# Optimization experiments

Measured on AMD Instinct MI355X. Metric: run time of the kernel, lower is better.

## Reference

```python
import jax, jax.numpy as jnp
import numpy as np

L = 5        # num_layer
D = 128      # emb_dim
N = 100000   # nodes
E = 500000   # edges
G = 128      # graphs in batch
NUM_TYPES = 100
NUM_ATTRS = 1000
MAX_DEPTH = 21


def _bn(x, g, b):
    # training-mode BatchNorm1d statistics (per-feature over rows)
    mu = x.mean(axis=0)
    var = x.var(axis=0)
    return (x - mu) * jax.lax.rsqrt(var + 1e-5) * g + b


def setup_inputs() -> dict:
    key = jax.random.key(0)
    ks = jax.random.split(key, 24)
    inp = {}
    x0 = jax.random.randint(ks[0], (N,), 0, NUM_TYPES)
    x1 = jax.random.randint(ks[1], (N,), 0, NUM_ATTRS)
    inp['x'] = jnp.stack([x0, x1], axis=1)
    inp['node_depth'] = jax.random.randint(ks[2], (N,), 0, MAX_DEPTH)
    inp['edge_index'] = jax.random.randint(ks[3], (2, E), 0, N)
    inp['batch'] = jnp.sort(jax.random.randint(ks[4], (N,), 0, G))
    inp['edge_attr'] = jax.random.normal(ks[5], (E, 2), dtype=jnp.float32)
    s = 0.02
    inp['type_emb'] = jax.random.normal(ks[6], (NUM_TYPES, D), dtype=jnp.float32) * s
    inp['attr_emb'] = jax.random.normal(ks[7], (NUM_ATTRS, D), dtype=jnp.float32) * s
    inp['depth_emb'] = jax.random.normal(ks[8], (MAX_DEPTH, D), dtype=jnp.float32) * s
    inp['vn_emb'] = jnp.zeros((1, D), dtype=jnp.float32)  # init constant 0
    inp['eps'] = jnp.zeros((L,), dtype=jnp.float32)       # GIN eps
    inp['edge_W'] = jax.random.normal(ks[9], (L, 2, D), dtype=jnp.float32) * s
    inp['edge_b'] = jnp.zeros((L, D), dtype=jnp.float32)
    inp['gin_W1'] = jax.random.normal(ks[10], (L, D, 2 * D), dtype=jnp.float32) * s
    inp['gin_b1'] = jnp.zeros((L, 2 * D), dtype=jnp.float32)
    inp['gin_bng'] = jnp.ones((L, 2 * D), dtype=jnp.float32)
    inp['gin_bnb'] = jnp.zeros((L, 2 * D), dtype=jnp.float32)
    inp['gin_W2'] = jax.random.normal(ks[11], (L, 2 * D, D), dtype=jnp.float32) * s
    inp['gin_b2'] = jnp.zeros((L, D), dtype=jnp.float32)
    inp['bng'] = jnp.ones((L, D), dtype=jnp.float32)
    inp['bnb'] = jnp.zeros((L, D), dtype=jnp.float32)
    inp['vn_W1'] = jax.random.normal(ks[12], (L - 1, D, 2 * D), dtype=jnp.float32) * s
    inp['vn_b1'] = jnp.zeros((L - 1, 2 * D), dtype=jnp.float32)
    inp['vn_bn1g'] = jnp.ones((L - 1, 2 * D), dtype=jnp.float32)
    inp['vn_bn1b'] = jnp.zeros((L - 1, 2 * D), dtype=jnp.float32)
    inp['vn_W2'] = jax.random.normal(ks[13], (L - 1, 2 * D, D), dtype=jnp.float32) * s
    inp['vn_b2'] = jnp.zeros((L - 1, D), dtype=jnp.float32)
    inp['vn_bn2g'] = jnp.ones((L - 1, D), dtype=jnp.float32)
    inp['vn_bn2b'] = jnp.zeros((L - 1, D), dtype=jnp.float32)
    return inp


def reference(x, node_depth, edge_index, batch, edge_attr,
              type_emb, attr_emb, depth_emb, vn_emb, eps,
              edge_W, edge_b, gin_W1, gin_b1, gin_bng, gin_bnb, gin_W2, gin_b2,
              bng, bnb, vn_W1, vn_b1, vn_bn1g, vn_bn1b, vn_W2, vn_b2, vn_bn2g, vn_bn2b):
    # node encoder: type + attribute + depth embeddings  -> [N, D]
    h = type_emb[x[:, 0]] + attr_emb[x[:, 1]] + depth_emb[node_depth]
    vn = jnp.broadcast_to(vn_emb[0], (G, D))  # virtual node per graph
    src, dst = edge_index[0], edge_index[1]
    for l in range(L):
        # broadcast virtual node to its graph's nodes
        h = h + vn[batch]
        # GIN conv: aggr_j relu(h_j + edge_emb), then (1+eps)*h + aggr -> MLP
        eemb = edge_attr @ edge_W[l] + edge_b[l]            # [E, D]
        msg = jax.nn.relu(h[src] + eemb)                    # [E, D]
        aggr = jax.ops.segment_sum(msg, dst, num_segments=N)
        z = (1.0 + eps[l]) * h + aggr
        z = jax.nn.relu(_bn(z @ gin_W1[l] + gin_b1[l], gin_bng[l], gin_bnb[l]))
        z = z @ gin_W2[l] + gin_b2[l]
        hn = _bn(z, bng[l], bnb[l])                         # outer BatchNorm
        if l < L - 1:
            hn = jax.nn.relu(hn)                            # dropout=identity (eval)
            # virtual node update: global_add_pool of pre-conv h + MLP
            vt = jax.ops.segment_sum(h, batch, num_segments=G) + vn
            vt = jax.nn.relu(_bn(vt @ vn_W1[l] + vn_b1[l], vn_bn1g[l], vn_bn1b[l]))
            vn = jax.nn.relu(_bn(vt @ vn_W2[l] + vn_b2[l], vn_bn2g[l], vn_bn2b[l]))
        h = hn
    return h  # JK == 'last'
```

## Files before the change

kernel.cpp:

```cpp
#include <hip/hip_runtime.h>

#define D 128
#define GG 128
#define SLOTS 64

typedef __attribute__((ext_vector_type(8))) short bf16x8;
typedef __attribute__((ext_vector_type(4))) float f32x4;

__device__ __forceinline__ short f2bf(float f) {
  unsigned u = __float_as_uint(f);
  unsigned r = u + 0x7fffu + ((u >> 16) & 1u);
  return (short)(r >> 16);
}
__device__ __forceinline__ float bf2f(unsigned short h) {
  return __uint_as_float(((unsigned)h) << 16);
}

__device__ __forceinline__ void bn_coef(float s, float q, float invn, float g, float b,
                                        float& sc, float& sh) {
  float mu = s * invn;
  float var = q * invn - mu * mu;
  sc = g * rsqrtf(var + 1e-5f);
  sh = b - mu * sc;
}

__global__ void k_deg(int E, const int* __restrict__ dst, int* __restrict__ deg) {
  int e = blockIdx.x * 256 + threadIdx.x;
  if (e < E) atomicAdd(&deg[dst[e]], 1);
}

__global__ void k_scan1(int N, const int* __restrict__ deg,
                        int* __restrict__ incl, int* __restrict__ blksum) {
  __shared__ int s[256];
  int t = threadIdx.x, n = blockIdx.x * 256 + t;
  int v = (n < N) ? ((deg[n] + 3) & ~3) : 0;
  s[t] = v; __syncthreads();
  for (int off = 1; off < 256; off <<= 1) {
    int x = (t >= off) ? s[t - off] : 0;
    __syncthreads();
    s[t] += x;
    __syncthreads();
  }
  if (n < N) incl[n] = s[t];
  if (t == 255) blksum[blockIdx.x] = s[255];
}

__global__ void k_scan2(int B, int* __restrict__ blksum) {
  __shared__ int s[512];
  int t = threadIdx.x;
  s[t] = (t < B) ? blksum[t] : 0;
  __syncthreads();
  for (int off = 1; off < 512; off <<= 1) {
    int x = (t >= off) ? s[t - off] : 0;
    __syncthreads();
    s[t] += x;
    __syncthreads();
  }
  if (t < B) blksum[t] = s[t];
}

__global__ void k_scan3(int N, const int* __restrict__ incl, const int* __restrict__ blksum,
                        const int* __restrict__ deg, int* __restrict__ row_ptr) {
  int n = blockIdx.x * 256 + threadIdx.x;
  if (n >= N) return;
  int b = n >> 8;
  int off = (b > 0) ? blksum[b - 1] : 0;
  int pdeg = (deg[n] + 3) & ~3;
  row_ptr[n] = off + incl[n] - pdeg;
  if (n == N - 1) row_ptr[N] = off + incl[n];
}

__global__ void k_fill(int E, const int* __restrict__ src, const int* __restrict__ dst,
                       const float* __restrict__ ea, const int* __restrict__ row_ptr,
                       int* __restrict__ cursor, int4* __restrict__ er) {
  int e = blockIdx.x * 256 + threadIdx.x;
  if (e >= E) return;
  int d = dst[e];
  int pos = row_ptr[d] + atomicAdd(&cursor[d], 1);
  er[pos] = make_int4(src[e] << 8, __float_as_int(ea[2 * e]), __float_as_int(ea[2 * e + 1]), 0);
}

__global__ void k_padfill(int N, const int* __restrict__ deg, const int* __restrict__ row_ptr,
                          int4* __restrict__ er) {
  int n = blockIdx.x * 256 + threadIdx.x;
  if (n >= N) return;
  int s = row_ptr[n] + deg[n], e = row_ptr[n + 1];
  int4 pad = make_int4(N << 8, 0, 0, 0);
  for (int p = s; p < e; ++p) er[p] = pad;
}

__global__ void k_sentinel(int N, short* __restrict__ h2) {
  h2[(size_t)N * D + threadIdx.x] = f2bf(-1e30f);
}

__global__ void k_pack(const float* __restrict__ gW1, const float* __restrict__ gW2,
                       short* __restrict__ w1t, short* __restrict__ w2t) {
  int id = blockIdx.x * 256 + threadIdx.x;
  if (id < 5 * 256 * 128) {
    int l = id / 32768, r = id % 32768, n = r / 128, k = r % 128;
    w1t[id] = f2bf(gW1[l * 32768 + k * 256 + n]);
  }
  if (id < 5 * 128 * 256) {
    int l = id / 32768, r = id % 32768, n = r / 256, k = r % 256;
    w2t[id] = f2bf(gW2[l * 32768 + k * 128 + n]);
  }
}

__global__ void k_coef(int NC,
                       const float* __restrict__ part_s, const float* __restrict__ part_q,
                       float* __restrict__ outs, float* __restrict__ outq) {
  int t = threadIdx.x;
  if (t >= NC) return;
  float s = 0.f, q = 0.f;
  #pragma unroll 4
  for (int i = 0; i < SLOTS; ++i) {
    s += part_s[i * NC + t];
    q += part_q[i * NC + t];
  }
  outs[t] = s; outq[t] = q;
}

__global__ void k_nodeprep(int N, int mode,
    const int* __restrict__ x, const int* __restrict__ depth,
    const float* __restrict__ te, const float* __restrict__ ae, const float* __restrict__ de,
    const short* __restrict__ z2, const float* __restrict__ s2, const float* __restrict__ q2,
    const float* __restrict__ g2, const float* __restrict__ b2,
    int vn_mode, const float* __restrict__ vne,
    const float* __restrict__ t2v, const float* __restrict__ vs2, const float* __restrict__ vq2,
    const float* __restrict__ vg2, const float* __restrict__ vb2,
    const int* __restrict__ batch,
    short* __restrict__ h2, float* __restrict__ vt_pool, int do_pool)
{
  int t = threadIdx.x;
  int d0 = (t & 63) * 2;
  int grp = t >> 6;
  int n0 = blockIdx.x * 32 + grp * 8;
  float invn = 1.0f / (float)N;
  float sc0 = 0.f, sh0 = 0.f, sc1 = 0.f, sh1 = 0.f;
  float vsc0 = 0.f, vsh0 = 0.f, vsc1 = 0.f, vsh1 = 0.f;
  if (mode == 1) {
    bn_coef(s2[d0], q2[d0], invn, g2[d0], b2[d0], sc0, sh0);
    bn_coef(s2[d0 + 1], q2[d0 + 1], invn, g2[d0 + 1], b2[d0 + 1], sc1, sh1);
  }
  if (vn_mode == 1) {
    bn_coef(vs2[d0], vq2[d0], 1.0f / (float)GG, vg2[d0], vb2[d0], vsc0, vsh0);
    bn_coef(vs2[d0 + 1], vq2[d0 + 1], 1.0f / (float)GG, vg2[d0 + 1], vb2[d0 + 1], vsc1, vsh1);
  }
  int cur = -1; float a0 = 0.f, a1 = 0.f;
  for (int k = 0; k < 8; ++k) {
    int n = n0 + k;
    if (n >= N) break;
    float h0, h1;
    if (mode == 0) {
      int x0 = x[2 * n], x1 = x[2 * n + 1], dp = depth[n];
      float2 e0 = *(const float2*)(te + (size_t)x0 * D + d0);
      float2 e1 = *(const float2*)(ae + (size_t)x1 * D + d0);
      float2 e2 = *(const float2*)(de + (size_t)dp * D + d0);
      h0 = e0.x + e1.x + e2.x;
      h1 = e0.y + e1.y + e2.y;
    } else {
      unsigned zv = *(const unsigned*)(z2 + (size_t)n * D + d0);
      h0 = fmaxf(bf2f((unsigned short)(zv & 0xffff)) * sc0 + sh0, 0.f);
      h1 = fmaxf(bf2f((unsigned short)(zv >> 16))    * sc1 + sh1, 0.f);
    }
    int g = batch[n];
    float v0, v1;
    if (vn_mode == 0) { v0 = vne[d0]; v1 = vne[d0 + 1]; }
    else {
      float2 tv = *(const float2*)(t2v + (size_t)g * D + d0);
      v0 = fmaxf(tv.x * vsc0 + vsh0, 0.f);
      v1 = fmaxf(tv.y * vsc1 + vsh1, 0.f);
    }
    h0 += v0; h1 += v1;
    unsigned o = ((unsigned)(unsigned short)f2bf(h0)) |
                 (((unsigned)(unsigned short)f2bf(h1)) << 16);
    *(unsigned*)(h2 + (size_t)n * D + d0) = o;
    if (do_pool) {
      if (g != cur) {
        if (cur >= 0) {
          atomicAdd(&vt_pool[cur * D + d0], a0);
          atomicAdd(&vt_pool[cur * D + d0 + 1], a1);
        }
        cur = g; a0 = 0.f; a1 = 0.f;
      }
      a0 += h0; a1 += h1;
    }
  }
  if (do_pool && cur >= 0) {
    atomicAdd(&vt_pool[cur * D + d0], a0);
    atomicAdd(&vt_pool[cur * D + d0 + 1], a1);
  }
}

__global__ void __launch_bounds__(256) k_gather(int N,
    const int* __restrict__ row_ptr, const int4* __restrict__ er,
    const float* __restrict__ ew, const float* __restrict__ eb,
    const float* __restrict__ epsp,
    const short* __restrict__ h2, short* __restrict__ am)
{
  int t = threadIdx.x;
  int w = t >> 6, l = t & 63;
  int n = blockIdx.x * 4 + w;
  if (n >= N) return;
  const char* h2b = (const char*)h2;
  int lb = l << 2;
  int d0 = l * 2;
  float ew00 = ew[d0], ew01 = ew[d0 + 1];
  float ew10 = ew[D + d0], ew11 = ew[D + d0 + 1];
  float eb0 = eb[d0], eb1 = eb[d0 + 1];
  float ep1 = 1.0f + epsp[0];
  unsigned hv = *(const unsigned*)(h2b + ((size_t)n << 8) + lb);
  float acc0 = ep1 * bf2f((unsigned short)(hv & 0xffff));
  float acc1 = ep1 * bf2f((unsigned short)(hv >> 16));
  int beg = row_ptr[n], end = row_ptr[n + 1];
  for (int i = beg; i < end; i += 4) {
    int4 e0 = er[i], e1 = er[i + 1], e2 = er[i + 2], e3 = er[i + 3];
    unsigned v0 = *(const unsigned*)(h2b + e0.x + lb);
    unsigned v1 = *(const unsigned*)(h2b + e1.x + lb);
    unsigned v2 = *(const unsigned*)(h2b + e2.x + lb);
    unsigned v3 = *(const unsigned*)(h2b + e3.x + lb);
    float a0x = __int_as_float(e0.y), a0y = __int_as_float(e0.z);
    float a1x = __int_as_float(e1.y), a1y = __int_as_float(e1.z);
    float a2x = __int_as_float(e2.y), a2y = __int_as_float(e2.z);
    float a3x = __int_as_float(e3.y), a3y = __int_as_float(e3.z);
    acc0 += fmaxf(bf2f((unsigned short)(v0 & 0xffff)) + a0x * ew00 + a0y * ew10 + eb0, 0.f);
    acc1 += fmaxf(bf2f((unsigned short)(v0 >> 16))    + a0x * ew01 + a0y * ew11 + eb1, 0.f);
    acc0 += fmaxf(bf2f((unsigned short)(v1 & 0xffff)) + a1x * ew00 + a1y * ew10 + eb0, 0.f);
    acc1 += fmaxf(bf2f((unsigned short)(v1 >> 16))    + a1x * ew01 + a1y * ew11 + eb1, 0.f);
    acc0 += fmaxf(bf2f((unsigned short)(v2 & 0xffff)) + a2x * ew00 + a2y * ew10 + eb0, 0.f);
    acc1 += fmaxf(bf2f((unsigned short)(v2 >> 16))    + a2x * ew01 + a2y * ew11 + eb1, 0.f);
    acc0 += fmaxf(bf2f((unsigned short)(v3 & 0xffff)) + a3x * ew00 + a3y * ew10 + eb0, 0.f);
    acc1 += fmaxf(bf2f((unsigned short)(v3 >> 16))    + a3x * ew01 + a3y * ew11 + eb1, 0.f);
  }
  unsigned o = ((unsigned)(unsigned short)f2bf(acc0)) |
               (((unsigned)(unsigned short)f2bf(acc1)) << 16);
  *(unsigned*)(am + (size_t)n * D + d0) = o;
}

template<int STAGES, int BN_A>
__global__ void __launch_bounds__(256, 4) k_gemm(int N, int NC, float invn,
    const short* __restrict__ A, int strideA,
    const short* __restrict__ Bt, int strideB,
    const float* __restrict__ bias,
    const float* __restrict__ pAs, const float* __restrict__ pAq,
    const float* __restrict__ gam, const float* __restrict__ bet,
    short* __restrict__ C, int strideC,
    float* __restrict__ part_s, float* __restrict__ part_q)
{
  __shared__ __align__(16) char As[32768];
  __shared__ float scs[256], shs[256];
  __shared__ float cs[128], cq[128];
  int t = threadIdx.x;
  int m0 = blockIdx.x * 128;
  int n0 = blockIdx.y * 128;
  int w = t >> 6, l = t & 63;
  int wr = w >> 1, wc = w & 1;
  int lm = l & 15, kb = l >> 4;

  if (t < 128) { cs[t] = 0.f; cq[t] = 0.f; }
  if (BN_A) {
    float s = 0.f, q = 0.f;
    #pragma unroll 8
    for (int i = 0; i < SLOTS; ++i) {
      s += pAs[i * 256 + t];
      q += pAq[i * 256 + t];
    }
    float a, c;
    bn_coef(s, q, invn, gam[t], bet[t], a, c);
    scs[t] = a; shs[t] = c;
  }
  __syncthreads();

  f32x4 acc[4][4];
  #pragma unroll
  for (int j = 0; j < 4; ++j) {
    float bj = bias[n0 + wc * 64 + j * 16 + lm];
    #pragma unroll
    for (int i = 0; i < 4; ++i) acc[i][j] = (f32x4){bj, bj, bj, bj};
  }

  #pragma unroll
  for (int s = 0; s < STAGES; ++s) {
    if (s > 0) __syncthreads();
    #pragma unroll
    for (int r = 0; r < 8; ++r) {
      int p = (r * 256 + t) * 16;
      int row = p >> 8, c = p & 255;
      int gr = m0 + row; if (gr > N - 1) gr = N - 1;
      bf16x8 v = *(const bf16x8*)((const char*)A + (size_t)gr * strideA + s * 256 + c);
      if (BN_A) {
        int kg = s * 128 + (c >> 1);
        float4 s0 = *(const float4*)(scs + kg);
        float4 s1 = *(const float4*)(scs + kg + 4);
        float4 h0 = *(const float4*)(shs + kg);
        float4 h1 = *(const float4*)(shs + kg + 4);
        v[0] = f2bf(fmaxf(bf2f((unsigned short)v[0]) * s0.x + h0.x, 0.f));
        v[1] = f2bf(fmaxf(bf2f((unsigned short)v[1]) * s0.y + h0.y, 0.f));
        v[2] = f2bf(fmaxf(bf2f((unsigned short)v[2]) * s0.z + h0.z, 0.f));
        v[3] = f2bf(fmaxf(bf2f((unsigned short)v[3]) * s0.w + h0.w, 0.f));
        v[4] = f2bf(fmaxf(bf2f((unsigned short)v[4]) * s1.x + h1.x, 0.f));
        v[5] = f2bf(fmaxf(bf2f((unsigned short)v[5]) * s1.y + h1.y, 0.f));
        v[6] = f2bf(fmaxf(bf2f((unsigned short)v[6]) * s1.z + h1.z, 0.f));
        v[7] = f2bf(fmaxf(bf2f((unsigned short)v[7]) * s1.w + h1.w, 0.f));
      }
      *(bf16x8*)(As + row * 256 + (c ^ ((row & 7) << 4))) = v;
    }
    __syncthreads();
    #pragma unroll
    for (int ks = 0; ks < 4; ++ks) {
      int kB = ks * 64 + kb * 16;
      bf16x8 fa[4], fb[4];
      #pragma unroll
      for (int j = 0; j < 4; ++j) {
        int cl = n0 + wc * 64 + j * 16 + lm;
        fb[j] = *(const bf16x8*)((const char*)Bt + (size_t)cl * strideB + s * 256 + kB);
      }
      #pragma unroll
      for (int i = 0; i < 4; ++i) {
        int rl = wr * 64 + i * 16 + lm;
        fa[i] = *(const bf16x8*)(As + rl * 256 + (kB ^ ((rl & 7) << 4)));
      }
      #pragma unroll
      for (int i = 0; i < 4; ++i)
        #pragma unroll
        for (int j = 0; j < 4; ++j)
          acc[i][j] = __builtin_amdgcn_mfma_f32_16x16x32_bf16(fa[i], fb[j], acc[i][j], 0, 0, 0);
    }
  }

  #pragma unroll
  for (int j = 0; j < 4; ++j) {
    int col = wc * 64 + j * 16 + lm;
    float sv = 0.f, qv = 0.f;
    #pragma unroll
    for (int i = 0; i < 4; ++i) {
      #pragma unroll
      for (int r = 0; r < 4; ++r) {
        int row = m0 + wr * 64 + i * 16 + kb * 4 + r;
        float vv = acc[i][j][r];
        if (row < N) { sv += vv; qv += vv * vv; }
      }
    }
    sv += __shfl_xor(sv, 16); sv += __shfl_xor(sv, 32);
    qv += __shfl_xor(qv, 16); qv += __shfl_xor(qv, 32);
    if (l < 16) { atomicAdd(&cs[col], sv); atomicAdd(&cq[col], qv); }
  }
  __syncthreads();
  if (t < 128) {
    int slot = (blockIdx.x + blockIdx.y) & (SLOTS - 1);
    atomicAdd(&part_s[(size_t)slot * NC + n0 + t], cs[t]);
    atomicAdd(&part_q[(size_t)slot * NC + n0 + t], cq[t]);
  }

  #pragma unroll
  for (int j = 0; j < 4; ++j) {
    int colb = (wc * 64 + j * 16 + lm) * 2;
    #pragma unroll
    for (int i = 0; i < 4; ++i) {
      int rowb = wr * 64 + i * 16 + kb * 4;
      #pragma unroll
      for (int r = 0; r < 4; ++r) {
        int row = rowb + r;
        *(short*)(As + row * 256 + (colb ^ ((row & 7) << 4))) = f2bf(acc[i][j][r]);
      }
    }
  }
  __syncthreads();
  {
    int tr = t >> 1, half = t & 1;
    int grow = m0 + tr;
    if (grow < N) {
      #pragma unroll
      for (int u = 0; u < 8; ++u) {
        int off = half * 128 + u * 16;
        bf16x8 v = *(const bf16x8*)(As + tr * 256 + (off ^ ((tr & 7) << 4)));
        *(bf16x8*)(C + (size_t)grow * strideC + n0 + half * 64 + u * 8) = v;
      }
    }
  }
}

__global__ void k_vn1(const float* __restrict__ vt_pool,
    int vn_mode, const float* __restrict__ vne, const float* __restrict__ t2v,
    const float* __restrict__ vs2, const float* __restrict__ vq2,
    const float* __restrict__ vg2, const float* __restrict__ vb2,
    const float* __restrict__ W1, const float* __restrict__ b1,
    float* __restrict__ t1v, float* __restrict__ s1, float* __restrict__ q1)
{
  __shared__ float vrow[128];
  int g = blockIdx.x, t = threadIdx.x;
  if (t < 128) {
    float vnv;
    if (vn_mode == 0) vnv = vne[t];
    else {
      float sc, sh;
      bn_coef(vs2[t], vq2[t], 1.f / (float)GG, vg2[t], vb2[t], sc, sh);
      vnv = fmaxf(t2v[g * D + t] * sc + sh, 0.f);
    }
    vrow[t] = vt_pool[g * D + t] + vnv;
  }
  __syncthreads();
  float acc = b1[t];
  for (int k = 0; k < 128; ++k) acc += vrow[k] * W1[k * 256 + t];
  t1v[g * 256 + t] = acc;
  atomicAdd(&s1[t], acc);
  atomicAdd(&q1[t], acc * acc);
}

__global__ void k_vn2(const float* __restrict__ t1v,
    const float* __restrict__ s1, const float* __restrict__ q1,
    const float* __restrict__ g1, const float* __restrict__ b1bn,
    const float* __restrict__ W2, const float* __restrict__ b2,
    float* __restrict__ t2v, float* __restrict__ s2, float* __restrict__ q2)
{
  __shared__ float p[256];
  int g = blockIdx.x, t = threadIdx.x;
  for (int u = t; u < 256; u += 128) {
    float sc, sh;
    bn_coef(s1[u], q1[u], 1.f / (float)GG, g1[u], b1bn[u], sc, sh);
    p[u] = fmaxf(t1v[g * 256 + u] * sc + sh, 0.f);
  }
  __syncthreads();
  float acc = b2[t];
  for (int k = 0; k < 256; ++k) acc += p[k] * W2[k * D + t];
  t2v[g * D + t] = acc;
  atomicAdd(&s2[t], acc);
  atomicAdd(&q2[t], acc * acc);
}

__global__ void k_out(int N, const short* __restrict__ z2,
    const float* __restrict__ s2, const float* __restrict__ q2,
    const float* __restrict__ g2, const float* __restrict__ b2, float* __restrict__ out)
{
  long long idx = (long long)blockIdx.x * 256 + threadIdx.x;
  long long base = idx * 2;
  if (base >= (long long)N * D) return;
  int d = (int)(base & (D - 1));
  float invn = 1.f / (float)N;
  unsigned v = *(const unsigned*)(z2 + base);
  float sc0, sh0, sc1, sh1;
  bn_coef(s2[d], q2[d], invn, g2[d], b2[d], sc0, sh0);
  bn_coef(s2[d + 1], q2[d + 1], invn, g2[d + 1], b2[d + 1], sc1, sh1);
  out[base]     = bf2f((unsigned short)(v & 0xffff)) * sc0 + sh0;
  out[base + 1] = bf2f((unsigned short)(v >> 16))    * sc1 + sh1;
}

extern "C" void kernel_launch(void* const* d_in, const int* in_sizes, int n_in,
                              void* d_out, int out_size, void* d_ws, size_t ws_size,
                              hipStream_t stream) {
  const int*   x     = (const int*)d_in[0];
  const int*   depth = (const int*)d_in[1];
  const int*   eidx  = (const int*)d_in[2];
  const int*   batch = (const int*)d_in[3];
  const float* ea    = (const float*)d_in[4];
  const float* te    = (const float*)d_in[5];
  const float* aemb  = (const float*)d_in[6];
  const float* de    = (const float*)d_in[7];
  const float* vne   = (const float*)d_in[8];
  const float* epsp  = (const float*)d_in[9];
  const float* eW    = (const float*)d_in[10];
  const float* eb    = (const float*)d_in[11];
  const float* gW1   = (const float*)d_in[12];
  const float* gb1   = (const float*)d_in[13];
  const float* gbng  = (const float*)d_in[14];
  const float* gbnb  = (const float*)d_in[15];
  const float* gW2   = (const float*)d_in[16];
  const float* gb2   = (const float*)d_in[17];
  const float* bng   = (const float*)d_in[18];
  const float* bnb   = (const float*)d_in[19];
  const float* vW1   = (const float*)d_in[20];
  const float* vb1   = (const float*)d_in[21];
  const float* vbn1g = (const float*)d_in[22];
  const float* vbn1b = (const float*)d_in[23];
  const float* vW2   = (const float*)d_in[24];
  const float* vb2   = (const float*)d_in[25];
  const float* vbn2g = (const float*)d_in[26];
  const float* vbn2b = (const float*)d_in[27];

  int N = in_sizes[0] / 2;
  int E = in_sizes[2] / 2;
  const int* src = eidx;
  const int* dst = eidx + E;

  char* wsp = (char*)d_ws;
  auto alloc = [&](size_t bytes) -> char* {
    char* p = wsp; wsp += (bytes + 15) & ~(size_t)15; return p;
  };
  short* h2         = (short*)alloc((size_t)(N + 1) * 128 * 2);
  short* am         = (short*)alloc((size_t)N * 128 * 2);
  short* t1         = (short*)alloc((size_t)N * 256 * 2);
  short* z2         = (short*)alloc((size_t)N * 128 * 2);
  short* w1t        = (short*)alloc((size_t)5 * 256 * 128 * 2);
  short* w2t        = (short*)alloc((size_t)5 * 128 * 256 * 2);
  int*   row_ptr    = (int*)alloc((size_t)(N + 1) * 4);
  int*   incl       = (int*)alloc((size_t)N * 4);
  int*   blksum     = (int*)alloc(512 * 4);
  int4*  er         = (int4*)alloc(((size_t)E + 3 * (size_t)N + 16) * 16);
  char* zero_base = wsp;
  int*  deg    = (int*)alloc((size_t)N * 4);
  int*  cursor = (int*)alloc((size_t)N * 4);
  float* sp = (float*)wsp;
  float *p1s[5], *p1q[5], *p2s[5], *p2q[5], *s2s[5], *q2s[5];
  for (int l = 0; l < 5; ++l) {
    p1s[l]=sp; sp+=SLOTS*256; p1q[l]=sp; sp+=SLOTS*256;
    p2s[l]=sp; sp+=SLOTS*128; p2q[l]=sp; sp+=SLOTS*128;
    s2s[l]=sp; sp+=128; q2s[l]=sp; sp+=128;
  }
  float *vt[4], *t1v[4], *t2v[4], *vs1[4], *vq1[4], *vs2[4], *vq2[4];
  for (int l = 0; l < 4; ++l) {
    vt[l]=sp;  sp+=GG*D;
    t1v[l]=sp; sp+=GG*256;
    t2v[l]=sp; sp+=GG*D;
    vs1[l]=sp; sp+=256; vq1[l]=sp; sp+=256;
    vs2[l]=sp; sp+=128; vq2[l]=sp; sp+=128;
  }
  size_t zero_bytes = (size_t)((char*)sp - zero_base);
  hipMemsetAsync(zero_base, 0, zero_bytes, stream);

  int eblk = (E + 255) / 256;
  int nblk = (N + 255) / 256;
  int B = nblk;
  k_deg<<<eblk, 256, 0, stream>>>(E, dst, deg);
  k_scan1<<<nblk, 256, 0, stream>>>(N, deg, incl, blksum);
  k_scan2<<<1, 512, 0, stream>>>(B, blksum);
  k_scan3<<<nblk, 256, 0, stream>>>(N, incl, blksum, deg, row_ptr);
  k_fill<<<eblk, 256, 0, stream>>>(E, src, dst, ea, row_ptr, cursor, er);
  k_padfill<<<nblk, 256, 0, stream>>>(N, deg, row_ptr, er);
  k_sentinel<<<1, 128, 0, stream>>>(N, h2);

  k_pack<<<(5 * 256 * 128 + 255) / 256, 256, 0, stream>>>(gW1, gW2, w1t, w2t);

  int nblk_a = (N + 31) / 32;
  int nblk_gth = (N + 3) / 4;
  int nblk_m = (N + 127) / 128;
  float invn = 1.f / (float)N;

  for (int l = 0; l < 5; ++l) {
    int mode    = (l == 0) ? 0 : 1;
    int vn_mode = (l == 0) ? 0 : 1;
    int do_pool = (l < 4) ? 1 : 0;
    const float* ps2  = (l > 0) ? s2s[l-1] : s2s[0];
    const float* pq2  = (l > 0) ? q2s[l-1] : q2s[0];
    const float* pg2  = (l > 0) ? bng + (l-1)*D : bng;
    const float* pb2  = (l > 0) ? bnb + (l-1)*D : bnb;
    const float* pt2v = (l > 0) ? t2v[l-1] : t2v[0];
    const float* pvs2 = (l > 0) ? vs2[l-1] : vs2[0];
    const float* pvq2 = (l > 0) ? vq2[l-1] : vq2[0];
    const float* pvg2 = (l > 0) ? vbn2g + (l-1)*D : vbn2g;
    const float* pvb2 = (l > 0) ? vbn2b + (l-1)*D : vbn2b;

    k_nodeprep<<<nblk_a, 256, 0, stream>>>(N, mode, x, depth, te, aemb, de,
        z2, ps2, pq2, pg2, pb2,
        vn_mode, vne, pt2v, pvs2, pvq2, pvg2, pvb2,
        batch, h2, do_pool ? vt[l] : vt[0], do_pool);

    k_gather<<<nblk_gth, 256, 0, stream>>>(N, row_ptr, er,
        eW + l*2*D, eb + l*D, epsp + l, h2, am);

    k_gemm<1, 0><<<dim3(nblk_m, 2), 256, 0, stream>>>(N, 256, invn,
        am, 256, w1t + (size_t)l*256*128, 256,
        gb1 + l*256, nullptr, nullptr, nullptr, nullptr,
        t1, 256, p1s[l], p1q[l]);

    k_gemm<2, 1><<<dim3(nblk_m, 1), 256, 0, stream>>>(N, 128, invn,
        t1, 512, w2t + (size_t)l*128*256, 512,
        gb2 + l*128, p1s[l], p1q[l], gbng + l*256, gbnb + l*256,
        z2, 128, p2s[l], p2q[l]);

    k_coef<<<1, 128, 0, stream>>>(128, p2s[l], p2q[l], s2s[l], q2s[l]);

    if (l < 4) {
      k_vn1<<<GG, 256, 0, stream>>>(vt[l], vn_mode, vne, pt2v, pvs2, pvq2, pvg2, pvb2,
          vW1 + (size_t)l*128*256, vb1 + l*256, t1v[l], vs1[l], vq1[l]);
      k_vn2<<<GG, 128, 0, stream>>>(t1v[l], vs1[l], vq1[l],
          vbn1g + l*256, vbn1b + l*256,
          vW2 + (size_t)l*256*128, vb2 + l*128, t2v[l], vs2[l], vq2[l]);
    }
  }

  k_out<<<(int)(((long long)N * D / 2 + 255) / 256), 256, 0, stream>>>(N, z2, s2s[4], q2s[4],
      bng + 4*D, bnb + 4*D, (float*)d_out);
}
```

Before: 987.0 us.

## Use direct global-to-LDS loads, register prefetch for BN path, coalesced output stores

For the non-BN GEMM path, A tiles are loaded straight into LDS with global_load_lds, applying the swizzle on the source address and skipping the register round trip. For the BN path, the next stage's A tile is prefetched into registers while the current stage is transformed. The epilogue store is remapped so 16 threads write each full row contiguously, giving coalesced global writes. The aim is fewer VGPR staging cycles and better overlap of memory latency, at the cost of extra registers for the prefetch buffer.

```diff
diff --git a/kernel.cpp b/kernel.cpp
--- a/kernel.cpp
+++ b/kernel.cpp
@@ -6,6 +6,8 @@
 
 typedef __attribute__((ext_vector_type(8))) short bf16x8;
 typedef __attribute__((ext_vector_type(4))) float f32x4;
+typedef __attribute__((address_space(1))) const unsigned gas_u32;
+typedef __attribute__((address_space(3))) unsigned las_u32;
 
 __device__ __forceinline__ short f2bf(float f) {
   unsigned u = __float_as_uint(f);
@@ -279,16 +281,36 @@
     for (int i = 0; i < 4; ++i) acc[i][j] = (f32x4){bj, bj, bj, bj};
   }
 
-  #pragma unroll
-  for (int s = 0; s < STAGES; ++s) {
-    if (s > 0) __syncthreads();
+  bf16x8 pre[8];
+  if (BN_A) {
     #pragma unroll
     for (int r = 0; r < 8; ++r) {
       int p = (r * 256 + t) * 16;
       int row = p >> 8, c = p & 255;
       int gr = m0 + row; if (gr > N - 1) gr = N - 1;
-      bf16x8 v = *(const bf16x8*)((const char*)A + (size_t)gr * strideA + s * 256 + c);
-      if (BN_A) {
+      pre[r] = *(const bf16x8*)((const char*)A + (size_t)gr * strideA + 0 * 256 + c);
+    }
+  }
+
+  #pragma unroll
+  for (int s = 0; s < STAGES; ++s) {
+    if (s > 0) __syncthreads();
+    if (!BN_A) {
+      #pragma unroll
+      for (int r = 0; r < 8; ++r) {
+        int p = (r * 256 + t) * 16;
+        int row = p >> 8, csw = p & 255;
+        int c = csw ^ ((row & 7) << 4);
+        int gr = m0 + row; if (gr > N - 1) gr = N - 1;
+        const char* gsrc = (const char*)A + (size_t)gr * strideA + s * 256 + c;
+        __builtin_amdgcn_global_load_lds((gas_u32*)gsrc, (las_u32*)(As + p), 16, 0, 0);
+      }
+    } else {
+      #pragma unroll
+      for (int r = 0; r < 8; ++r) {
+        int p = (r * 256 + t) * 16;
+        int row = p >> 8, c = p & 255;
+        bf16x8 v = pre[r];
         int kg = s * 128 + (c >> 1);
         float4 s0 = *(const float4*)(scs + kg);
         float4 s1 = *(const float4*)(scs + kg + 4);
@@ -302,8 +324,17 @@
         v[5] = f2bf(fmaxf(bf2f((unsigned short)v[5]) * s1.y + h1.y, 0.f));
         v[6] = f2bf(fmaxf(bf2f((unsigned short)v[6]) * s1.z + h1.z, 0.f));
         v[7] = f2bf(fmaxf(bf2f((unsigned short)v[7]) * s1.w + h1.w, 0.f));
-      }
-      *(bf16x8*)(As + row * 256 + (c ^ ((row & 7) << 4))) = v;
+        *(bf16x8*)(As + row * 256 + (c ^ ((row & 7) << 4))) = v;
+      }
+      if (s + 1 < STAGES) {
+        #pragma unroll
+        for (int r = 0; r < 8; ++r) {
+          int p = (r * 256 + t) * 16;
+          int row = p >> 8, c = p & 255;
+          int gr = m0 + row; if (gr > N - 1) gr = N - 1;
+          pre[r] = *(const bf16x8*)((const char*)A + (size_t)gr * strideA + (s + 1) * 256 + c);
+        }
+      }
     }
     __syncthreads();
     #pragma unroll
@@ -367,15 +398,15 @@
   }
   __syncthreads();
   {
-    int tr = t >> 1, half = t & 1;
-    int grow = m0 + tr;
-    if (grow < N) {
-      #pragma unroll
-      for (int u = 0; u < 8; ++u) {
-        int off = half * 128 + u * 16;
-        bf16x8 v = *(const bf16x8*)(As + tr * 256 + (off ^ ((tr & 7) << 4)));
-        *(bf16x8*)(C + (size_t)grow * strideC + n0 + half * 64 + u * 8) = v;
-      }
+    int rr = t >> 4, ck = t & 15;
+    #pragma unroll
+    for (int it = 0; it < 8; ++it) {
+      int row = it * 16 + rr;
+      int grow = m0 + row;
+      int off = ck * 16;
+      bf16x8 v = *(const bf16x8*)(As + row * 256 + (off ^ ((row & 7) << 4)));
+      if (grow < N)
+        *(bf16x8*)(C + (size_t)grow * strideC + n0 + ck * 8) = v;
     }
   }
 }
```

After: 1.018 ms. 1.03x slower.

## Retile MLP GEMMs to 64-row full-width blocks and fuse virtual-node kernels

Applied to the files above, without the earlier changes.

The first GEMM now computes all 256 output columns per 64-row block, so each A tile is read once instead of once per column half. The second GEMM also drops to 64-row tiles, which roughly doubles the block count. The BN coefficients for the hidden layer are now computed once in a separate k_coef launch rather than re-reduced from 64 slots in every GEMM block. The two virtual-node MLP kernels are merged into one, with an atomic-counter grid barrier across 128 blocks. That merge relies on all blocks being co-resident and adds a spin-wait, and it also adds one extra small kernel launch per layer.

```diff
diff --git a/kernel.cpp b/kernel.cpp
--- a/kernel.cpp
+++ b/kernel.cpp
@@ -106,8 +106,10 @@
   }
 }
 
-__global__ void k_coef(int NC,
+__global__ void k_coef(int NC, float invn,
                        const float* __restrict__ part_s, const float* __restrict__ part_q,
+                       const float* __restrict__ g, const float* __restrict__ b,
+                       float* __restrict__ sc, float* __restrict__ sh,
                        float* __restrict__ outs, float* __restrict__ outq) {
   int t = threadIdx.x;
   if (t >= NC) return;
@@ -117,7 +119,12 @@
     s += part_s[i * NC + t];
     q += part_q[i * NC + t];
   }
-  outs[t] = s; outq[t] = q;
+  if (outs) { outs[t] = s; outq[t] = q; }
+  if (g) {
+    float a, c;
+    bn_coef(s, q, invn, g[t], b[t], a, c);
+    sc[t] = a; sh[t] = c;
+  }
 }
 
 __global__ void k_nodeprep(int N, int mode,
@@ -237,91 +244,184 @@
   *(unsigned*)(am + (size_t)n * D + d0) = o;
 }
 
-template<int STAGES, int BN_A>
-__global__ void __launch_bounds__(256, 4) k_gemm(int N, int NC, float invn,
-    const short* __restrict__ A, int strideA,
-    const short* __restrict__ Bt, int strideB,
+__global__ void __launch_bounds__(256) k_gemm1(int N,
+    const short* __restrict__ A, const short* __restrict__ Bt,
     const float* __restrict__ bias,
-    const float* __restrict__ pAs, const float* __restrict__ pAq,
-    const float* __restrict__ gam, const float* __restrict__ bet,
-    short* __restrict__ C, int strideC,
+    short* __restrict__ C,
     float* __restrict__ part_s, float* __restrict__ part_q)
 {
-  __shared__ __align__(16) char As[32768];
+  __shared__ __align__(16) char As[16384];
+  __shared__ float cs[256], cq[256];
+  int t = threadIdx.x;
+  int m0 = blockIdx.x * 64;
+  int w = t >> 6, l = t & 63;
+  int wr = w >> 1, wc = w & 1;
+  int lm = l & 15, kb = l >> 4;
+  cs[t] = 0.f; cq[t] = 0.f;
+
+  f32x4 acc[2][8];
+  #pragma unroll
+  for (int j = 0; j < 8; ++j) {
+    float bj = bias[wc * 128 + j * 16 + lm];
+    acc[0][j] = (f32x4){bj, bj, bj, bj};
+    acc[1][j] = (f32x4){bj, bj, bj, bj};
+  }
+
+  #pragma unroll
+  for (int r = 0; r < 4; ++r) {
+    int p = (r * 256 + t) * 16;
+    int row = p >> 8, c = p & 255;
+    int gr = m0 + row; if (gr > N - 1) gr = N - 1;
+    bf16x8 v = *(const bf16x8*)((const char*)A + (size_t)gr * 256 + c);
+    *(bf16x8*)(As + row * 256 + (c ^ ((row & 7) << 4))) = v;
+  }
+  __syncthreads();
+  #pragma unroll
+  for (int ks = 0; ks < 4; ++ks) {
+    int kB = ks * 64 + kb * 16;
+    bf16x8 fa[2], fb[8];
+    #pragma unroll
+    for (int j = 0; j < 8; ++j) {
+      int cl = wc * 128 + j * 16 + lm;
+      fb[j] = *(const bf16x8*)((const char*)Bt + (size_t)cl * 256 + kB);
+    }
+    #pragma unroll
+    for (int i = 0; i < 2; ++i) {
+      int rl = wr * 32 + i * 16 + lm;
+      fa[i] = *(const bf16x8*)(As + rl * 256 + (kB ^ ((rl & 7) << 4)));
+    }
+    #pragma unroll
+    for (int i = 0; i < 2; ++i)
+      #pragma unroll
+      for (int j = 0; j < 8; ++j)
+        acc[i][j] = __builtin_amdgcn_mfma_f32_16x16x32_bf16(fa[i], fb[j], acc[i][j], 0, 0, 0);
+  }
+
+  #pragma unroll
+  for (int j = 0; j < 8; ++j) {
+    int col = wc * 128 + j * 16 + lm;
+    float sv = 0.f, qv = 0.f;
+    #pragma unroll
+    for (int i = 0; i < 2; ++i) {
+      #pragma unroll
+      for (int r = 0; r < 4; ++r) {
+        int row = m0 + wr * 32 + i * 16 + kb * 4 + r;
+        float vv = acc[i][j][r];
+        if (row < N) { sv += vv; qv += vv * vv; }
+      }
+    }
+    sv += __shfl_xor(sv, 16); sv += __shfl_xor(sv, 32);
+    qv += __shfl_xor(qv, 16); qv += __shfl_xor(qv, 32);
+    if (l < 16) { atomicAdd(&cs[col], sv); atomicAdd(&cq[col], qv); }
+  }
+  __syncthreads();
+  {
+    int slot = blockIdx.x & (SLOTS - 1);
+    atomicAdd(&part_s[(size_t)slot * 256 + t], cs[t]);
+    atomicAdd(&part_q[(size_t)slot * 256 + t], cq[t]);
+  }
+
+  #pragma unroll
+  for (int hf = 0; hf < 2; ++hf) {
+    __syncthreads();
+    if (wc == hf) {
+      #pragma unroll
+      for (int j = 0; j < 8; ++j) {
+        int colb = (j * 16 + lm) * 2;
+        #pragma unroll
+        for (int i = 0; i < 2; ++i) {
+          int rowb = wr * 32 + i * 16 + kb * 4;
+          #pragma unroll
+          for (int r = 0; r < 4; ++r) {
+            int row = rowb + r;
+            *(short*)(As + row * 256 + (colb ^ ((row & 7) << 4))) = f2bf(acc[i][j][r]);
+          }
+        }
+      }
+    }
+    __syncthreads();
+    int row = t >> 2, quad = t & 3;
+    int grow = m0 + row;
+    if (grow < N) {
+      #pragma unroll
+      for (int u = 0; u < 4; ++u) {
+        int chunk = quad * 4 + u;
+        int off = chunk * 16;
+        bf16x8 v = *(const bf16x8*)(As + row * 256 + (off ^ ((row & 7) << 4)));
+        *(bf16x8*)(C + (size_t)grow * 256 + hf * 128 + chunk * 8) = v;
+      }
+    }
+  }
+}
+
+__global__ void __launch_bounds__(256) k_gemm2(int N,
+    const short* __restrict__ A, const short* __restrict__ Bt,
+    const float* __restrict__ bias,
+    const float* __restrict__ scA, const float* __restrict__ shA,
+    short* __restrict__ C,
+    float* __restrict__ part_s, float* __restrict__ part_q)
+{
+  __shared__ __align__(16) char As[16384];
   __shared__ float scs[256], shs[256];
   __shared__ float cs[128], cq[128];
   int t = threadIdx.x;
-  int m0 = blockIdx.x * 128;
-  int n0 = blockIdx.y * 128;
+  int m0 = blockIdx.x * 64;
   int w = t >> 6, l = t & 63;
   int wr = w >> 1, wc = w & 1;
   int lm = l & 15, kb = l >> 4;
-
   if (t < 128) { cs[t] = 0.f; cq[t] = 0.f; }
-  if (BN_A) {
-    float s = 0.f, q = 0.f;
-    #pragma unroll 8
-    for (int i = 0; i < SLOTS; ++i) {
-      s += pAs[i * 256 + t];
-      q += pAq[i * 256 + t];
-    }
-    float a, c;
-    bn_coef(s, q, invn, gam[t], bet[t], a, c);
-    scs[t] = a; shs[t] = c;
-  }
-  __syncthreads();
-
-  f32x4 acc[4][4];
+  scs[t] = scA[t]; shs[t] = shA[t];
+  __syncthreads();
+
+  f32x4 acc[2][4];
   #pragma unroll
   for (int j = 0; j < 4; ++j) {
-    float bj = bias[n0 + wc * 64 + j * 16 + lm];
-    #pragma unroll
-    for (int i = 0; i < 4; ++i) acc[i][j] = (f32x4){bj, bj, bj, bj};
-  }
-
-  #pragma unroll
-  for (int s = 0; s < STAGES; ++s) {
+    float bj = bias[wc * 64 + j * 16 + lm];
+    acc[0][j] = (f32x4){bj, bj, bj, bj};
+    acc[1][j] = (f32x4){bj, bj, bj, bj};
+  }
+
+  #pragma unroll
+  for (int s = 0; s < 2; ++s) {
     if (s > 0) __syncthreads();
     #pragma unroll
-    for (int r = 0; r < 8; ++r) {
+    for (int r = 0; r < 4; ++r) {
       int p = (r * 256 + t) * 16;
       int row = p >> 8, c = p & 255;
       int gr = m0 + row; if (gr > N - 1) gr = N - 1;
-      bf16x8 v = *(const bf16x8*)((const char*)A + (size_t)gr * strideA + s * 256 + c);
-      if (BN_A) {
-        int kg = s * 128 + (c >> 1);
-        float4 s0 = *(const float4*)(scs + kg);
-        float4 s1 = *(const float4*)(scs + kg + 4);
-        float4 h0 = *(const float4*)(shs + kg);
-        float4 h1 = *(const float4*)(shs + kg + 4);
-        v[0] = f2bf(fmaxf(bf2f((unsigned short)v[0]) * s0.x + h0.x, 0.f));
-        v[1] = f2bf(fmaxf(bf2f((unsigned short)v[1]) * s0.y + h0.y, 0.f));
-        v[2] = f2bf(fmaxf(bf2f((unsigned short)v[2]) * s0.z + h0.z, 0.f));
-        v[3] = f2bf(fmaxf(bf2f((unsigned short)v[3]) * s0.w + h0.w, 0.f));
-        v[4] = f2bf(fmaxf(bf2f((unsigned short)v[4]) * s1.x + h1.x, 0.f));
-        v[5] = f2bf(fmaxf(bf2f((unsigned short)v[5]) * s1.y + h1.y, 0.f));
-        v[6] = f2bf(fmaxf(bf2f((unsigned short)v[6]) * s1.z + h1.z, 0.f));
-        v[7] = f2bf(fmaxf(bf2f((unsigned short)v[7]) * s1.w + h1.w, 0.f));
-      }
+      bf16x8 v = *(const bf16x8*)((const char*)A + (size_t)gr * 512 + s * 256 + c);
+      int kg = s * 128 + (c >> 1);
+      float4 s0 = *(const float4*)(scs + kg);
+      float4 s1 = *(const float4*)(scs + kg + 4);
+      float4 h0 = *(const float4*)(shs + kg);
+      float4 h1 = *(const float4*)(shs + kg + 4);
+      v[0] = f2bf(fmaxf(bf2f((unsigned short)v[0]) * s0.x + h0.x, 0.f));
+      v[1] = f2bf(fmaxf(bf2f((unsigned short)v[1]) * s0.y + h0.y, 0.f));
+      v[2] = f2bf(fmaxf(bf2f((unsigned short)v[2]) * s0.z + h0.z, 0.f));
+      v[3] = f2bf(fmaxf(bf2f((unsigned short)v[3]) * s0.w + h0.w, 0.f));
+      v[4] = f2bf(fmaxf(bf2f((unsigned short)v[4]) * s1.x + h1.x, 0.f));
+      v[5] = f2bf(fmaxf(bf2f((unsigned short)v[5]) * s1.y + h1.y, 0.f));
+      v[6] = f2bf(fmaxf(bf2f((unsigned short)v[6]) * s1.z + h1.z, 0.f));
+      v[7] = f2bf(fmaxf(bf2f((unsigned short)v[7]) * s1.w + h1.w, 0.f));
       *(bf16x8*)(As + row * 256 + (c ^ ((row & 7) << 4))) = v;
     }
     __syncthreads();
     #pragma unroll
     for (int ks = 0; ks < 4; ++ks) {
       int kB = ks * 64 + kb * 16;
-      bf16x8 fa[4], fb[4];
+      bf16x8 fa[2], fb[4];
       #pragma unroll
       for (int j = 0; j < 4; ++j) {
-        int cl = n0 + wc * 64 + j * 16 + lm;
-        fb[j] = *(const bf16x8*)((const char*)Bt + (size_t)cl * strideB + s * 256 + kB);
-      }
-      #pragma unroll
-      for (int i = 0; i < 4; ++i) {
-        int rl = wr * 64 + i * 16 + lm;
+        int cl = wc * 64 + j * 16 + lm;
+        fb[j] = *(const bf16x8*)((const char*)Bt + (size_t)cl * 512 + s * 256 + kB);
+      }
+      #pragma unroll
+      for (int i = 0; i < 2; ++i) {
+        int rl = wr * 32 + i * 16 + lm;
         fa[i] = *(const bf16x8*)(As + rl * 256 + (kB ^ ((rl & 7) << 4)));
       }
       #pragma unroll
-      for (int i = 0; i < 4; ++i)
+      for (int i = 0; i < 2; ++i)
         #pragma unroll
         for (int j = 0; j < 4; ++j)
           acc[i][j] = __builtin_amdgcn_mfma_f32_16x16x32_bf16(fa[i], fb[j], acc[i][j], 0, 0, 0);
@@ -333,10 +433,10 @@
     int col = wc * 64 + j * 16 + lm;
     float sv = 0.f, qv = 0.f;
     #pragma unroll
-    for (int i = 0; i < 4; ++i) {
+    for (int i = 0; i < 2; ++i) {
       #pragma unroll
       for (int r = 0; r < 4; ++r) {
-        int row = m0 + wr * 64 + i * 16 + kb * 4 + r;
+        int row = m0 + wr * 32 + i * 16 + kb * 4 + r;
         float vv = acc[i][j][r];
         if (row < N) { sv += vv; qv += vv * vv; }
       }
@@ -347,17 +447,17 @@
   }
   __syncthreads();
   if (t < 128) {
-    int slot = (blockIdx.x + blockIdx.y) & (SLOTS - 1);
-    atomicAdd(&part_s[(size_t)slot * NC + n0 + t], cs[t]);
-    atomicAdd(&part_q[(size_t)slot * NC + n0 + t], cq[t]);
+    int slot = blockIdx.x & (SLOTS - 1);
+    atomicAdd(&part_s[(size_t)slot * 128 + t], cs[t]);
+    atomicAdd(&part_q[(size_t)slot * 128 + t], cq[t]);
   }
 
   #pragma unroll
   for (int j = 0; j < 4; ++j) {
     int colb = (wc * 64 + j * 16 + lm) * 2;
     #pragma unroll
-    for (int i = 0; i < 4; ++i) {
-      int rowb = wr * 64 + i * 16 + kb * 4;
+    for (int i = 0; i < 2; ++i) {
+      int rowb = wr * 32 + i * 16 + kb * 4;
       #pragma unroll
       for (int r = 0; r < 4; ++r) {
         int row = rowb + r;
@@ -367,65 +467,73 @@
   }
   __syncthreads();
   {
-    int tr = t >> 1, half = t & 1;
-    int grow = m0 + tr;
+    int row = t >> 2, quad = t & 3;
+    int grow = m0 + row;
     if (grow < N) {
       #pragma unroll
-      for (int u = 0; u < 8; ++u) {
-        int off = half * 128 + u * 16;
-        bf16x8 v = *(const bf16x8*)(As + tr * 256 + (off ^ ((tr & 7) << 4)));
-        *(bf16x8*)(C + (size_t)grow * strideC + n0 + half * 64 + u * 8) = v;
-      }
-    }
-  }
-}
-
-__global__ void k_vn1(const float* __restrict__ vt_pool,
-    int vn_mode, const float* __restrict__ vne, const float* __restrict__ t2v,
-    const float* __restrict__ vs2, const float* __restrict__ vq2,
-    const float* __restrict__ vg2, const float* __restrict__ vb2,
+      for (int u = 0; u < 4; ++u) {
+        int chunk = quad * 4 + u;
+        int off = chunk * 16;
+        bf16x8 v = *(const bf16x8*)(As + row * 256 + (off ^ ((row & 7) << 4)));
+        *(bf16x8*)(C + (size_t)grow * 128 + chunk * 8) = v;
+      }
+    }
+  }
+}
+
+__global__ void k_vn12(const float* __restrict__ vt_pool,
+    int vn_mode, const float* __restrict__ vne, const float* __restrict__ t2v_prev,
+    const float* __restrict__ pvs2, const float* __restrict__ pvq2,
+    const float* __restrict__ pvg2, const float* __restrict__ pvb2,
     const float* __restrict__ W1, const float* __restrict__ b1,
-    float* __restrict__ t1v, float* __restrict__ s1, float* __restrict__ q1)
+    const float* __restrict__ g1bn, const float* __restrict__ b1bn,
+    const float* __restrict__ W2, const float* __restrict__ b2,
+    float* __restrict__ t2v,
+    float* __restrict__ s1, float* __restrict__ q1,
+    float* __restrict__ s2, float* __restrict__ q2,
+    int* __restrict__ cnt)
 {
   __shared__ float vrow[128];
+  __shared__ float p[256];
   int g = blockIdx.x, t = threadIdx.x;
   if (t < 128) {
     float vnv;
     if (vn_mode == 0) vnv = vne[t];
     else {
       float sc, sh;
-      bn_coef(vs2[t], vq2[t], 1.f / (float)GG, vg2[t], vb2[t], sc, sh);
-      vnv = fmaxf(t2v[g * D + t] * sc + sh, 0.f);
+      bn_coef(pvs2[t], pvq2[t], 1.f / (float)GG, pvg2[t], pvb2[t], sc, sh);
+      vnv = fmaxf(t2v_prev[g * D + t] * sc + sh, 0.f);
     }
     vrow[t] = vt_pool[g * D + t] + vnv;
   }
   __syncthreads();
-  float acc = b1[t];
-  for (int k = 0; k < 128; ++k) acc += vrow[k] * W1[k * 256 + t];
-  t1v[g * 256 + t] = acc;
-  atomicAdd(&s1[t], acc);
-  atomicAdd(&q1[t], acc * acc);
-}
-
-__global__ void k_vn2(const float* __restrict__ t1v,
-    const float* __restrict__ s1, const float* __restrict__ q1,
-    const float* __restrict__ g1, const float* __restrict__ b1bn,
-    const float* __restrict__ W2, const float* __restrict__ b2,
-    float* __restrict__ t2v, float* __restrict__ s2, float* __restrict__ q2)
-{
-  __shared__ float p[256];
-  int g = blockIdx.x, t = threadIdx.x;
-  for (int u = t; u < 256; u += 128) {
+  float acc1 = b1[t];
+  for (int k = 0; k < 128; ++k) acc1 += vrow[k] * W1[k * 256 + t];
+  atomicAdd(&s1[t], acc1);
+  atomicAdd(&q1[t], acc1 * acc1);
+  __syncthreads();
+  if (t == 0) {
+    __threadfence();
+    atomicAdd(cnt, 1);
+    while (__hip_atomic_load(cnt, __ATOMIC_ACQUIRE, __HIP_MEMORY_SCOPE_AGENT) < GG)
+      __builtin_amdgcn_s_sleep(2);
+  }
+  __syncthreads();
+  {
+    float ss = __hip_atomic_load(&s1[t], __ATOMIC_RELAXED, __HIP_MEMORY_SCOPE_AGENT);
+    float qq = __hip_atomic_load(&q1[t], __ATOMIC_RELAXED, __HIP_MEMORY_SCOPE_AGENT);
     float sc, sh;
-    bn_coef(s1[u], q1[u], 1.f / (float)GG, g1[u], b1bn[u], sc, sh);
-    p[u] = fmaxf(t1v[g * 256 + u] * sc + sh, 0.f);
-  }
-  __syncthreads();
-  float acc = b2[t];
-  for (int k = 0; k < 256; ++k) acc += p[k] * W2[k * D + t];
-  t2v[g * D + t] = acc;
-  atomicAdd(&s2[t], acc);
-  atomicAdd(&q2[t], acc * acc);
+    bn_coef(ss, qq, 1.f / (float)GG, g1bn[t], b1bn[t], sc, sh);
+    p[t] = fmaxf(acc1 * sc + sh, 0.f);
+  }
+  __syncthreads();
+  if (t < 128) {
+    float acc2 = b2[t];
+    for (int k = 0; k < 256; ++k) acc2 += p[k] * W2[k * D + t];
+    t2v[g * D + t] = acc2;
+    atomicAdd(&s2[t], acc2);
+    atomicAdd(&q2[t], acc2 * acc2);
+  }
 }
 
 __global__ void k_out(int N, const short* __restrict__ z2,
@@ -496,9 +604,12 @@
   int*   incl       = (int*)alloc((size_t)N * 4);
   int*   blksum     = (int*)alloc(512 * 4);
   int4*  er         = (int4*)alloc(((size_t)E + 3 * (size_t)N + 16) * 16);
+  float* sc1        = (float*)alloc(256 * 4);
+  float* sh1        = (float*)alloc(256 * 4);
   char* zero_base = wsp;
   int*  deg    = (int*)alloc((size_t)N * 4);
   int*  cursor = (int*)alloc((size_t)N * 4);
+  int*  vncnt  = (int*)alloc(8 * 4);
   float* sp = (float*)wsp;
   float *p1s[5], *p1q[5], *p2s[5], *p2q[5], *s2s[5], *q2s[5];
   for (int l = 0; l < 5; ++l) {
@@ -506,10 +617,9 @@
     p2s[l]=sp; sp+=SLOTS*128; p2q[l]=sp; sp+=SLOTS*128;
     s2s[l]=sp; sp+=128; q2s[l]=sp; sp+=128;
   }
-  float *vt[4], *t1v[4], *t2v[4], *vs1[4], *vq1[4], *vs2[4], *vq2[4];
+  float *vt[4], *t2v[4], *vs1[4], *vq1[4], *vs2[4], *vq2[4];
   for (int l = 0; l < 4; ++l) {
     vt[l]=sp;  sp+=GG*D;
-    t1v[l]=sp; sp+=GG*256;
     t2v[l]=sp; sp+=GG*D;
     vs1[l]=sp; sp+=256; vq1[l]=sp; sp+=256;
     vs2[l]=sp; sp+=128; vq2[l]=sp; sp+=128;
@@ -532,7 +642,7 @@
 
   int nblk_a = (N + 31) / 32;
   int nblk_gth = (N + 3) / 4;
-  int nblk_m = (N + 127) / 128;
+  int nblk_m = (N + 63) / 64;
   float invn = 1.f / (float)N;
 
   for (int l = 0; l < 5; ++l) {
@@ -557,24 +667,25 @@
     k_gather<<<nblk_gth, 256, 0, stream>>>(N, row_ptr, er,
         eW + l*2*D, eb + l*D, epsp + l, h2, am);
 
-    k_gemm<1, 0><<<dim3(nblk_m, 2), 256, 0, stream>>>(N, 256, invn,
-        am, 256, w1t + (size_t)l*256*128, 256,
-        gb1 + l*256, nullptr, nullptr, nullptr, nullptr,
-        t1, 256, p1s[l], p1q[l]);
-
-    k_gemm<2, 1><<<dim3(nblk_m, 1), 256, 0, stream>>>(N, 128, invn,
-        t1, 512, w2t + (size_t)l*128*256, 512,
-        gb2 + l*128, p1s[l], p1q[l], gbng + l*256, gbnb + l*256,
-        z2, 128, p2s[l], p2q[l]);
-
-    k_coef<<<1, 128, 0, stream>>>(128, p2s[l], p2q[l], s2s[l], q2s[l]);
+    k_gemm1<<<nblk_m, 256, 0, stream>>>(N,
+        am, w1t + (size_t)l*256*128, gb1 + l*256, t1, p1s[l], p1q[l]);
+
+    k_coef<<<1, 256, 0, stream>>>(256, invn, p1s[l], p1q[l],
+        gbng + l*256, gbnb + l*256, sc1, sh1, nullptr, nullptr);
+
+    k_gemm2<<<nblk_m, 256, 0, stream>>>(N,
+        t1, w2t + (size_t)l*128*256, gb2 + l*128, sc1, sh1, z2, p2s[l], p2q[l]);
+
+    k_coef<<<1, 128, 0, stream>>>(128, invn, p2s[l], p2q[l],
+        nullptr, nullptr, nullptr, nullptr, s2s[l], q2s[l]);
 
     if (l < 4) {
-      k_vn1<<<GG, 256, 0, stream>>>(vt[l], vn_mode, vne, pt2v, pvs2, pvq2, pvg2, pvb2,
-          vW1 + (size_t)l*128*256, vb1 + l*256, t1v[l], vs1[l], vq1[l]);
-      k_vn2<<<GG, 128, 0, stream>>>(t1v[l], vs1[l], vq1[l],
+      k_vn12<<<GG, 256, 0, stream>>>(vt[l], vn_mode, vne, pt2v,
+          pvs2, pvq2, pvg2, pvb2,
+          vW1 + (size_t)l*128*256, vb1 + l*256,
           vbn1g + l*256, vbn1b + l*256,
-          vW2 + (size_t)l*256*128, vb2 + l*128, t2v[l], vs2[l], vq2[l]);
+          vW2 + (size_t)l*256*128, vb2 + l*128,
+          t2v[l], vs1[l], vq1[l], vs2[l], vq2[l], vncnt + l);
     }
   }
 
```

Result: slower. 1.190 ms (+20.5%).

## Stage B tile in LDS and write GEMM output directly from registers

Applied to the files above, without the earlier changes.

Loads the B tile into a swizzled shared-memory buffer per stage, so the MFMA fragments for B come from LDS instead of strided global loads. Drops the LDS-staged epilogue and instead stores each bf16 output element straight from the accumulators to global memory. Also lowers the launch-bounds occupancy hint from 4 to 2 and reduces the unroll of the partial-sum reduction. The extra 32KB of LDS lowers occupancy, and the direct epilogue issues scattered 2-byte stores in place of coalesced 16-byte stores.

```diff
diff --git a/kernel.cpp b/kernel.cpp
--- a/kernel.cpp
+++ b/kernel.cpp
@@ -238,16 +238,17 @@
 }
 
 template<int STAGES, int BN_A>
-__global__ void __launch_bounds__(256, 4) k_gemm(int N, int NC, float invn,
+__global__ void __launch_bounds__(256, 2) k_gemm(int N, int NC, float invn,
     const short* __restrict__ A, int strideA,
     const short* __restrict__ Bt, int strideB,
     const float* __restrict__ bias,
     const float* __restrict__ pAs, const float* __restrict__ pAq,
-    const float* __restrict__ gam, const float* __restrict__ bet,
+    const float* __restrict__ g1, const float* __restrict__ b1,
     short* __restrict__ C, int strideC,
     float* __restrict__ part_s, float* __restrict__ part_q)
 {
   __shared__ __align__(16) char As[32768];
+  __shared__ __align__(16) char Bs[32768];
   __shared__ float scs[256], shs[256];
   __shared__ float cs[128], cq[128];
   int t = threadIdx.x;
@@ -260,13 +261,13 @@
   if (t < 128) { cs[t] = 0.f; cq[t] = 0.f; }
   if (BN_A) {
     float s = 0.f, q = 0.f;
-    #pragma unroll 8
+    #pragma unroll 4
     for (int i = 0; i < SLOTS; ++i) {
       s += pAs[i * 256 + t];
       q += pAq[i * 256 + t];
     }
     float a, c;
-    bn_coef(s, q, invn, gam[t], bet[t], a, c);
+    bn_coef(s, q, invn, g1[t], b1[t], a, c);
     scs[t] = a; shs[t] = c;
   }
   __syncthreads();
@@ -305,20 +306,27 @@
       }
       *(bf16x8*)(As + row * 256 + (c ^ ((row & 7) << 4))) = v;
     }
+    #pragma unroll
+    for (int r = 0; r < 8; ++r) {
+      int p = (r * 256 + t) * 16;
+      int col = p >> 8, c = p & 255;
+      bf16x8 v = *(const bf16x8*)((const char*)Bt + (size_t)(n0 + col) * strideB + s * 256 + c);
+      *(bf16x8*)(Bs + col * 256 + (c ^ ((col & 7) << 4))) = v;
+    }
     __syncthreads();
     #pragma unroll
     for (int ks = 0; ks < 4; ++ks) {
       int kB = ks * 64 + kb * 16;
       bf16x8 fa[4], fb[4];
       #pragma unroll
-      for (int j = 0; j < 4; ++j) {
-        int cl = n0 + wc * 64 + j * 16 + lm;
-        fb[j] = *(const bf16x8*)((const char*)Bt + (size_t)cl * strideB + s * 256 + kB);
-      }
-      #pragma unroll
       for (int i = 0; i < 4; ++i) {
         int rl = wr * 64 + i * 16 + lm;
         fa[i] = *(const bf16x8*)(As + rl * 256 + (kB ^ ((rl & 7) << 4)));
+      }
+      #pragma unroll
+      for (int j = 0; j < 4; ++j) {
+        int cl = wc * 64 + j * 16 + lm;
+        fb[j] = *(const bf16x8*)(Bs + cl * 256 + (kB ^ ((cl & 7) << 4)));
       }
       #pragma unroll
       for (int i = 0; i < 4; ++i)
@@ -330,7 +338,7 @@
 
   #pragma unroll
   for (int j = 0; j < 4; ++j) {
-    int col = wc * 64 + j * 16 + lm;
+    int col = n0 + wc * 64 + j * 16 + lm;
     float sv = 0.f, qv = 0.f;
     #pragma unroll
     for (int i = 0; i < 4; ++i) {
@@ -338,45 +346,18 @@
       for (int r = 0; r < 4; ++r) {
         int row = m0 + wr * 64 + i * 16 + kb * 4 + r;
         float vv = acc[i][j][r];
-        if (row < N) { sv += vv; qv += vv * vv; }
+        if (row < N) { C[(size_t)row * strideC + col] = f2bf(vv); sv += vv; qv += vv * vv; }
       }
     }
     sv += __shfl_xor(sv, 16); sv += __shfl_xor(sv, 32);
     qv += __shfl_xor(qv, 16); qv += __shfl_xor(qv, 32);
-    if (l < 16) { atomicAdd(&cs[col], sv); atomicAdd(&cq[col], qv); }
+    if (l < 16) { atomicAdd(&cs[col - n0], sv); atomicAdd(&cq[col - n0], qv); }
   }
   __syncthreads();
   if (t < 128) {
     int slot = (blockIdx.x + blockIdx.y) & (SLOTS - 1);
     atomicAdd(&part_s[(size_t)slot * NC + n0 + t], cs[t]);
     atomicAdd(&part_q[(size_t)slot * NC + n0 + t], cq[t]);
-  }
-
-  #pragma unroll
-  for (int j = 0; j < 4; ++j) {
-    int colb = (wc * 64 + j * 16 + lm) * 2;
-    #pragma unroll
-    for (int i = 0; i < 4; ++i) {
-      int rowb = wr * 64 + i * 16 + kb * 4;
-      #pragma unroll
-      for (int r = 0; r < 4; ++r) {
-        int row = rowb + r;
-        *(short*)(As + row * 256 + (colb ^ ((row & 7) << 4))) = f2bf(acc[i][j][r]);
-      }
-    }
-  }
-  __syncthreads();
-  {
-    int tr = t >> 1, half = t & 1;
-    int grow = m0 + tr;
-    if (grow < N) {
-      #pragma unroll
-      for (int u = 0; u < 8; ++u) {
-        int off = half * 128 + u * 16;
-        bf16x8 v = *(const bf16x8*)(As + tr * 256 + (off ^ ((tr & 7) << 4)));
-        *(bf16x8*)(C + (size_t)grow * strideC + n0 + half * 64 + u * 8) = v;
-      }
-    }
   }
 }
 
```

New measurement: 903.9 us. 8.4% less time.
